# Optimization experiments

Measured on AMD Instinct MI355X. Metric: run time of the kernel, lower is better.

## Reference

```python
import jax, jax.numpy as jnp
import numpy as np

EPS = 1e-8          # torch CosineSimilarity eps
TEMPERATURE = 0.5
N = 4096            # device_size (== batch_size, world_size=1)
D = 256             # projection embedding dim


def setup_inputs() -> dict:
    key = jax.random.key(0)
    k1, k2 = jax.random.split(key)
    return {
        "z_i": jax.random.normal(k1, (N, D), dtype=jnp.float32),
        "z_j": jax.random.normal(k2, (N, D), dtype=jnp.float32),
    }


def reference(z_i, z_j):
    n = z_i.shape[0]
    # z_large = [z_i ; z_j]  (world_size == 1 layout)
    z = jnp.concatenate([z_i, z_j], axis=0)                      # [2N, D]
    zn = z / jnp.maximum(jnp.linalg.norm(z, axis=1, keepdims=True), EPS)
    zi_n, zj_n = zn[:n], zn[n:]
    # cosine similarity via normalize + GEMM (same math as CosineSimilarity(dim=2))
    sim_i = (zi_n @ zn.T) / TEMPERATURE                          # [N, 2N]
    sim_j = (zj_n @ zn.T) / TEMPERATURE                          # [N, 2N]
    idx = jnp.arange(n)
    neg_inf = jnp.finfo(sim_i.dtype).min
    # positives: sim_i row i vs column N+i; sim_j row i vs column i
    pos_i = sim_i[idx, n + idx]                                  # [N]
    pos_j = sim_j[idx, idx]                                      # [N]
    # exclude self-similarity from the softmax denominator
    sim_i_m = sim_i.at[idx, idx].set(neg_inf)
    sim_j_m = sim_j.at[idx, n + idx].set(neg_inf)
    # CrossEntropyLoss(sum) with label 0 on [pos, negs] == sum(lse - pos)
    lse_i = jax.scipy.special.logsumexp(sim_i_m, axis=1)
    lse_j = jax.scipy.special.logsumexp(sim_j_m, axis=1)
    loss_i = jnp.sum(lse_i - pos_i) / n
    loss_j = jnp.sum(lse_j - pos_j) / n
    return loss_i, loss_j
```

## Files before the change

### kernel.cpp

```cpp
#include <hip/hip_runtime.h>

#define NN   4096
#define TWON 8192
#define DD   256
#define TINV 2.0f
#define SCALE 1.69864363f
#define CS   16

typedef __attribute__((ext_vector_type(8)))  short v8s;
typedef __attribute__((ext_vector_type(16))) float v16f;

__device__ inline unsigned short f2bf(float f) {
  unsigned int u = __float_as_uint(f);
  u += 0x7FFFu + ((u >> 16) & 1u);
  return (unsigned short)(u >> 16);
}

__global__ void k_normpos(const float* __restrict__ zi, const float* __restrict__ zj,
                          unsigned short* __restrict__ zn, float* __restrict__ pospart) {
  int wid = threadIdx.x >> 6, lane = threadIdx.x & 63;
  int pr  = blockIdx.x * 2 + (wid >> 1);
  int isj = wid & 1;
  const float* src = (isj ? zj : zi) + (size_t)pr * DD;
  float4 v = *(const float4*)(src + lane * 4);
  float ss = v.x*v.x + v.y*v.y + v.z*v.z + v.w*v.w;
  #pragma unroll
  for (int m = 1; m < 64; m <<= 1) ss += __shfl_xor(ss, m, 64);
  float nrm = fmaxf(sqrtf(ss), 1e-8f);

  __shared__ float zbuf[2][DD];
  __shared__ float nbuf[2];
  if (!isj) {
    *(float4*)&zbuf[wid >> 1][lane * 4] = v;
    if (lane == 0) nbuf[wid >> 1] = nrm;
  }

  float sc = SCALE / nrm;
  ushort4 o;
  o.x = f2bf(v.x * sc); o.y = f2bf(v.y * sc);
  o.z = f2bf(v.z * sc); o.w = f2bf(v.w * sc);
  int zrow = (isj ? NN : 0) + pr;
  *(ushort4*)(zn + (size_t)zrow * DD + lane * 4) = o;

  __syncthreads();
  if (isj) {
    float4 a = *(const float4*)&zbuf[wid >> 1][lane * 4];
    float d = a.x*v.x + a.y*v.y + a.z*v.z + a.w*v.w;
    #pragma unroll
    for (int m = 1; m < 64; m <<= 1) d += __shfl_xor(d, m, 64);
    if (lane == 0) pospart[pr] = d * TINV / (nbuf[wid >> 1] * nrm);
  }
}

__global__ __launch_bounds__(256, 2) void k_main(const unsigned short* __restrict__ zn,
                                                 float* __restrict__ wsum) {
  const char* znb = (const char*)zn;
  int tid = threadIdx.x, wid = tid >> 6, lane = tid & 63;
  int rb = blockIdx.x >> 4, cs = blockIdx.x & 15;
  int wrow0 = rb * 256 + wid * 64;
  int lr = lane & 31, lg = lane >> 5;
  int cbase = cs * 512;
  int lane_src = lr * 512 + lg * 16;

  v8s afrag[2][16];
  #pragma unroll
  for (int h = 0; h < 2; ++h) {
    #pragma unroll
    for (int kk = 0; kk < 16; ++kk) {
      size_t off = (size_t)(wrow0 + h * 32 + lr) * 512 + kk * 32 + lg * 16;
      afrag[h][kk] = *(const v8s*)(znb + off);
    }
  }

  __shared__ char tile0[16384];
  __shared__ char tile1[16384];
  v16f sumv0, sumv1;
  #pragma unroll
  for (int q = 0; q < 16; ++q) { sumv0[q] = 0.f; sumv1[q] = 0.f; }

#define STAGE(CT, BUF) { \
    size_t gb = (size_t)(cbase + (CT) * 32) * 512; \
    _Pragma("unroll") \
    for (int p = 0; p < 4; ++p) { \
      int t = wid * 4 + p; \
      const char* s = znb + gb + t * 32 + lane_src; \
      __builtin_amdgcn_global_load_lds((const __attribute__((address_space(1))) void*)s, \
          (__attribute__((address_space(3))) void*)&(BUF)[t * 1024], 16, 0, 0); \
    } }

#define COMPUTE(BUF, CT) { \
    int ctile = cbase + (CT) * 32; \
    v16f acc0, acc1; \
    _Pragma("unroll") \
    for (int q = 0; q < 16; ++q) { acc0[q] = 0.f; acc1[q] = 0.f; } \
    const char* bb = &(BUF)[lg * 512 + lr * 16]; \
    _Pragma("unroll") \
    for (int kk = 0; kk < 16; ++kk) { \
      v8s b = *(const v8s*)(bb + kk * 1024); \
      acc0 = __builtin_amdgcn_mfma_f32_32x32x16_bf16(afrag[0][kk], b, acc0, 0, 0, 0); \
      acc1 = __builtin_amdgcn_mfma_f32_32x32x16_bf16(afrag[1][kk], b, acc1, 0, 0, 0); \
    } \
    if (ctile == wrow0 || ctile == wrow0 + 32) { \
      bool h0 = (ctile == wrow0); \
      _Pragma("unroll") \
      for (int q = 0; q < 16; ++q) { \
        int ro = 4 * lg + (q & 3) + 8 * (q >> 2); \
        float e0 = __builtin_amdgcn_exp2f(acc0[q]); \
        float e1 = __builtin_amdgcn_exp2f(acc1[q]); \
        if (h0 && ro == lr) e0 = 0.f; \
        if (!h0 && ro == lr) e1 = 0.f; \
        sumv0[q] += e0; sumv1[q] += e1; \
      } \
    } else { \
      _Pragma("unroll") \
      for (int q = 0; q < 16; ++q) { \
        sumv0[q] += __builtin_amdgcn_exp2f(acc0[q]); \
        sumv1[q] += __builtin_amdgcn_exp2f(acc1[q]); \
      } \
    } }

  STAGE(0, tile0);
  __syncthreads();
  for (int c2 = 0; c2 < 8; ++c2) {
    int ctB = c2 * 2 + 1;
    STAGE(ctB, tile1);
    COMPUTE(tile0, c2 * 2);
    __syncthreads();
    if (ctB + 1 < 16) STAGE(ctB + 1, tile0);
    COMPUTE(tile1, ctB);
    __syncthreads();
  }
#undef STAGE
#undef COMPUTE

  #pragma unroll
  for (int q = 0; q < 16; ++q) {
    float v0 = sumv0[q], v1 = sumv1[q];
    #pragma unroll
    for (int m = 1; m < 32; m <<= 1) {
      v0 += __shfl_xor(v0, m, 64);
      v1 += __shfl_xor(v1, m, 64);
    }
    sumv0[q] = v0; sumv1[q] = v1;
  }
  if (lr < 16) {
    int qi = lr;
    float o0 = 0.f, o1 = 0.f;
    #pragma unroll
    for (int q = 0; q < 16; ++q) {
      o0 = (q == qi) ? sumv0[q] : o0;
      o1 = (q == qi) ? sumv1[q] : o1;
    }
    int ro = 4 * lg + (qi & 3) + 8 * (qi >> 2);
    wsum[(size_t)(wrow0 + ro) * CS + cs] = o0;
    wsum[(size_t)(wrow0 + 32 + ro) * CS + cs] = o1;
  }
}

__global__ void k_lse(const float* __restrict__ wsum, float* __restrict__ lsepart) {
  int tid = threadIdx.x;
  int row = blockIdx.x * 128 + tid;
  const float4* p = (const float4*)(wsum + (size_t)row * 16);
  float4 a = p[0], b = p[1], c = p[2], d = p[3];
  float s = (((a.x + a.y) + (a.z + a.w)) + ((b.x + b.y) + (b.z + b.w)))
          + (((c.x + c.y) + (c.z + c.w)) + ((d.x + d.y) + (d.z + d.w)));
  float lse = logf(s);
  #pragma unroll
  for (int m = 1; m < 64; m <<= 1) lse += __shfl_xor(lse, m, 64);
  __shared__ float sb[2];
  if ((tid & 63) == 0) sb[tid >> 6] = lse;
  __syncthreads();
  if (tid == 0) lsepart[blockIdx.x] = sb[0] + sb[1];
}

__global__ void k_final(const float* __restrict__ lsepart, const float* __restrict__ pospart,
                        float* __restrict__ out) {
  int tid = threadIdx.x, wid = tid >> 6, lane = tid & 63;
  float li = (tid < 32) ? lsepart[tid] : 0.f;
  float lj = (tid >= 32 && tid < 64) ? lsepart[tid] : 0.f;
  float pp = 0.f;
  #pragma unroll
  for (int k = 0; k < 16; ++k) pp += pospart[tid + 256 * k];
  #pragma unroll
  for (int m = 1; m < 64; m <<= 1) {
    li += __shfl_xor(li, m, 64);
    lj += __shfl_xor(lj, m, 64);
    pp += __shfl_xor(pp, m, 64);
  }
  __shared__ float sI[4], sJ[4], sP[4];
  if (lane == 0) { sI[wid] = li; sJ[wid] = lj; sP[wid] = pp; }
  __syncthreads();
  if (tid == 0) {
    float SI = (sI[0] + sI[1]) + (sI[2] + sI[3]);
    float SJ = (sJ[0] + sJ[1]) + (sJ[2] + sJ[3]);
    float SP = (sP[0] + sP[1]) + (sP[2] + sP[3]);
    out[0] = (SI - SP) * (1.0f / NN);
    out[1] = (SJ - SP) * (1.0f / NN);
  }
}

extern "C" void kernel_launch(void* const* d_in, const int* in_sizes, int n_in,
                              void* d_out, int out_size, void* d_ws, size_t ws_size,
                              hipStream_t stream) {
  const float* zi = (const float*)d_in[0];
  const float* zj = (const float*)d_in[1];
  float* out = (float*)d_out;
  char* ws = (char*)d_ws;
  unsigned short* zn = (unsigned short*)ws;
  float* pospart = (float*)(ws + 4194304);
  float* lsepart = (float*)(ws + 4210688);
  float* wsum    = (float*)(ws + 4210944);

  k_normpos<<<2048, 256, 0, stream>>>(zi, zj, zn, pospart);
  k_main<<<512, 256, 0, stream>>>(zn, wsum);
  k_lse<<<64, 128, 0, stream>>>(wsum, lsepart);
  k_final<<<1, 256, 0, stream>>>(lsepart, pospart, out);
}
```

Measured before the change: 53.91 us.

## Use 4-buffer LDS ring with 3-deep prefetch and one barrier per tile

Replaces the double-buffered LDS staging in the main GEMM+exp kernel with a four-slot ring buffer that keeps three tiles in flight. Explicit vmcnt waits and a single s_barrier per iteration replace two __syncthreads per pair of tiles, and the MFMA loop runs at raised wave priority. The goal is to hide global-to-LDS latency and cut barrier overhead. LDS use doubles to 64KB per block, which may limit occupancy at two blocks per CU.

```diff
diff --git a/kernel.cpp b/kernel.cpp
--- a/kernel.cpp
+++ b/kernel.cpp
@@ -72,66 +72,71 @@
     }
   }
 
-  __shared__ char tile0[16384];
-  __shared__ char tile1[16384];
+  __shared__ char tiles[4][16384];
   v16f sumv0, sumv1;
   #pragma unroll
   for (int q = 0; q < 16; ++q) { sumv0[q] = 0.f; sumv1[q] = 0.f; }
 
-#define STAGE(CT, BUF) { \
+#define STAGE(CT, BI) { \
     size_t gb = (size_t)(cbase + (CT) * 32) * 512; \
     _Pragma("unroll") \
     for (int p = 0; p < 4; ++p) { \
-      int t = wid * 4 + p; \
-      const char* s = znb + gb + t * 32 + lane_src; \
-      __builtin_amdgcn_global_load_lds((const __attribute__((address_space(1))) void*)s, \
-          (__attribute__((address_space(3))) void*)&(BUF)[t * 1024], 16, 0, 0); \
+      int ti = wid * 4 + p; \
+      const char* sp = znb + gb + ti * 32 + lane_src; \
+      __builtin_amdgcn_global_load_lds((const __attribute__((address_space(1))) void*)sp, \
+          (__attribute__((address_space(3))) void*)&tiles[BI][ti * 1024], 16, 0, 0); \
     } }
 
-#define COMPUTE(BUF, CT) { \
-    int ctile = cbase + (CT) * 32; \
-    v16f acc0, acc1; \
-    _Pragma("unroll") \
-    for (int q = 0; q < 16; ++q) { acc0[q] = 0.f; acc1[q] = 0.f; } \
-    const char* bb = &(BUF)[lg * 512 + lr * 16]; \
-    _Pragma("unroll") \
-    for (int kk = 0; kk < 16; ++kk) { \
-      v8s b = *(const v8s*)(bb + kk * 1024); \
-      acc0 = __builtin_amdgcn_mfma_f32_32x32x16_bf16(afrag[0][kk], b, acc0, 0, 0, 0); \
-      acc1 = __builtin_amdgcn_mfma_f32_32x32x16_bf16(afrag[1][kk], b, acc1, 0, 0, 0); \
-    } \
-    if (ctile == wrow0 || ctile == wrow0 + 32) { \
-      bool h0 = (ctile == wrow0); \
-      _Pragma("unroll") \
-      for (int q = 0; q < 16; ++q) { \
-        int ro = 4 * lg + (q & 3) + 8 * (q >> 2); \
-        float e0 = __builtin_amdgcn_exp2f(acc0[q]); \
-        float e1 = __builtin_amdgcn_exp2f(acc1[q]); \
-        if (h0 && ro == lr) e0 = 0.f; \
-        if (!h0 && ro == lr) e1 = 0.f; \
-        sumv0[q] += e0; sumv1[q] += e1; \
-      } \
-    } else { \
-      _Pragma("unroll") \
-      for (int q = 0; q < 16; ++q) { \
-        sumv0[q] += __builtin_amdgcn_exp2f(acc0[q]); \
-        sumv1[q] += __builtin_amdgcn_exp2f(acc1[q]); \
-      } \
-    } }
-
-  STAGE(0, tile0);
-  __syncthreads();
-  for (int c2 = 0; c2 < 8; ++c2) {
-    int ctB = c2 * 2 + 1;
-    STAGE(ctB, tile1);
-    COMPUTE(tile0, c2 * 2);
-    __syncthreads();
-    if (ctB + 1 < 16) STAGE(ctB + 1, tile0);
-    COMPUTE(tile1, ctB);
-    __syncthreads();
+  STAGE(0, 0);
+  STAGE(1, 1);
+  STAGE(2, 2);
+
+  #pragma unroll 1
+  for (int t = 0; t < 16; ++t) {
+    if (t <= 13)      asm volatile("s_waitcnt vmcnt(8)" ::: "memory");
+    else if (t == 14) asm volatile("s_waitcnt vmcnt(4)" ::: "memory");
+    else              asm volatile("s_waitcnt vmcnt(0)" ::: "memory");
+    __builtin_amdgcn_sched_barrier(0);
+    __builtin_amdgcn_s_barrier();
+    __builtin_amdgcn_sched_barrier(0);
+
+    if (t + 3 < 16) { STAGE(t + 3, ((t + 3) & 3)); }
+
+    int bi = t & 3;
+    int ctile = cbase + t * 32;
+    v16f acc0, acc1;
+    #pragma unroll
+    for (int q = 0; q < 16; ++q) { acc0[q] = 0.f; acc1[q] = 0.f; }
+    const char* bb = &tiles[bi][lg * 512 + lr * 16];
+    __builtin_amdgcn_s_setprio(1);
+    #pragma unroll
+    for (int kk = 0; kk < 16; ++kk) {
+      v8s b = *(const v8s*)(bb + kk * 1024);
+      acc0 = __builtin_amdgcn_mfma_f32_32x32x16_bf16(afrag[0][kk], b, acc0, 0, 0, 0);
+      acc1 = __builtin_amdgcn_mfma_f32_32x32x16_bf16(afrag[1][kk], b, acc1, 0, 0, 0);
+    }
+    __builtin_amdgcn_s_setprio(0);
+
+    if (ctile == wrow0 || ctile == wrow0 + 32) {
+      bool h0 = (ctile == wrow0);
+      #pragma unroll
+      for (int q = 0; q < 16; ++q) {
+        int ro = 4 * lg + (q & 3) + 8 * (q >> 2);
+        float e0 = __builtin_amdgcn_exp2f(acc0[q]);
+        float e1 = __builtin_amdgcn_exp2f(acc1[q]);
+        if (h0 && ro == lr) e0 = 0.f;
+        if (!h0 && ro == lr) e1 = 0.f;
+        sumv0[q] += e0; sumv1[q] += e1;
+      }
+    } else {
+      #pragma unroll
+      for (int q = 0; q < 16; ++q) {
+        sumv0[q] += __builtin_amdgcn_exp2f(acc0[q]);
+        sumv1[q] += __builtin_amdgcn_exp2f(acc1[q]);
+      }
+    }
   }
 #undef STAGE
-#undef COMPUTE
 
   #pragma unroll
   for (int q = 0; q < 16; ++q) {
@@ -160,7 +165,7 @@
 __global__ void k_lse(const float* __restrict__ wsum, float* __restrict__ lsepart) {
   int tid = threadIdx.x;
   int row = blockIdx.x * 128 + tid;
-  const float4* p = (const float4*)(wsum + (size_t)row * 16);
+  const float4* p = (const float4*)(wsum + (size_t)row * CS);
   float4 a = p[0], b = p[1], c = p[2], d = p[3];
   float s = (((a.x + a.y) + (a.z + a.w)) + ((b.x + b.y) + (b.z + b.w)))
           + (((c.x + c.y) + (c.z + c.w)) + ((d.x + d.y) + (d.z + d.w)));
```

Result: no change. 54.95 us (+1.9%).
